# Optimization experiments

Measured on AMD Instinct MI355X. Metric: run time of the kernel, lower is better.

The kernel has to match this reference:

```python
import jax, jax.numpy as jnp
import numpy as np

N_NODES = 100000
N_EDGES = 1600000
IN_CH = 128
OUT_CH = 32
HEADS = 2
NEG_SLOPE = 0.2  # GATv2Conv default negative_slope


def setup_inputs() -> dict:
    key = jax.random.key(0)
    ks = jax.random.split(key, 6)
    x = jax.random.normal(ks[0], (N_NODES, IN_CH), dtype=jnp.float32)
    edge_index = jax.random.randint(ks[1], (2, N_EDGES), 0, N_NODES, dtype=jnp.int64)
    s_in = 1.0 / np.sqrt(IN_CH)
    Wl = jax.random.normal(ks[2], (IN_CH, HEADS * OUT_CH), dtype=jnp.float32) * s_in  # lin_l weight
    Wr = jax.random.normal(ks[3], (IN_CH, HEADS * OUT_CH), dtype=jnp.float32) * s_in  # lin_r weight
    bl = jnp.zeros((HEADS * OUT_CH,), dtype=jnp.float32)
    br = jnp.zeros((HEADS * OUT_CH,), dtype=jnp.float32)
    att = jax.random.normal(ks[4], (HEADS, OUT_CH), dtype=jnp.float32) * (1.0 / np.sqrt(OUT_CH))
    bias = jnp.zeros((OUT_CH,), dtype=jnp.float32)  # output bias (concat=False -> size out_channels)
    return {"x": x, "Wl": Wl, "bl": bl, "Wr": Wr, "br": br, "att": att, "bias": bias,
            "edge_index": edge_index}


def _gatv2_layer(x, Wl, bl, Wr, br, att, bias, edge_index):
    N = x.shape[0]
    H, C = att.shape
    # add self loops (GATv2Conv default add_self_loops=True)
    loops = jnp.arange(N, dtype=edge_index.dtype)
    src = jnp.concatenate([edge_index[0], loops])  # [E+N] message sources j
    dst = jnp.concatenate([edge_index[1], loops])  # [E+N] message targets i
    # per-node linear transforms (share_weights=False)
    xl = (x @ Wl + bl).reshape(N, H, C)
    xr = (x @ Wr + br).reshape(N, H, C)
    # GATv2 dynamic attention: a^T LeakyReLU(xl[j] + xr[i])
    h = xl[src] + xr[dst]                                   # [E, H, C]
    e = jnp.einsum('ehc,hc->eh', jax.nn.leaky_relu(h, NEG_SLOPE), att)  # [E, H]
    # segment softmax over incoming edges of each target node
    m = jax.ops.segment_max(e, dst, num_segments=N)         # [N, H]
    a = jnp.exp(e - m[dst])
    denom = jax.ops.segment_sum(a, dst, num_segments=N)     # [N, H]
    alpha = a / (denom[dst] + 1e-16)                        # [E, H]
    # weighted scatter-add of source messages
    out = jax.ops.segment_sum(alpha[:, :, None] * xl[src], dst, num_segments=N)  # [N, H, C]
    out = out.mean(axis=1) + bias                           # concat=False -> head mean
    return jax.nn.silu(out)                                 # activation='silu'


def reference(x, Wl, bl, Wr, br, att, bias, edge_index):
    return _gatv2_layer(x, Wl, bl, Wr, br, att, bias, edge_index)
```

## Files before the change

### kernel.cpp

```cpp
#include <hip/hip_runtime.h>
#include <math.h>

#define BSH 9
#define BMASK ((1 << BSH) - 1)
#define CAP 12288
#define ACH 8192

typedef unsigned int uint;
typedef __attribute__((ext_vector_type(8))) short bf16x8;
typedef __attribute__((ext_vector_type(4))) float f32x4;
typedef __attribute__((ext_vector_type(2))) float f32x2;

static __device__ __forceinline__ unsigned short f2bf(float f) {
    uint u = __float_as_uint(f);
    return (unsigned short)((u + 0x7fffu + ((u >> 16) & 1u)) >> 16);
}

static __device__ __forceinline__ bf16x8 pack8(f32x4 a, f32x4 b) {
    uint p0, p1, p2, p3;
    asm("v_cvt_pk_bf16_f32 %0, %1, %2" : "=v"(p0) : "v"(a.x), "v"(a.y));
    asm("v_cvt_pk_bf16_f32 %0, %1, %2" : "=v"(p1) : "v"(a.z), "v"(a.w));
    asm("v_cvt_pk_bf16_f32 %0, %1, %2" : "=v"(p2) : "v"(b.x), "v"(b.y));
    asm("v_cvt_pk_bf16_f32 %0, %1, %2" : "=v"(p3) : "v"(b.z), "v"(b.w));
    uint4 u = make_uint4(p0, p1, p2, p3);
    return *(bf16x8*)&u;
}

static __device__ __forceinline__ uint pk2(float a, float b) {
    uint d;
    asm("v_cvt_pk_bf16_f32 %0, %1, %2" : "=v"(d) : "v"(a), "v"(b));
    return d;
}

static __device__ __forceinline__ f32x2 dec2(uint u) {
    f32x2 r;
    r.x = __uint_as_float(u << 16);
    r.y = __uint_as_float(u & 0xffff0000u);
    return r;
}

static __device__ __forceinline__ f32x2 abs2(f32x2 h) {
    f32x2 r;
    r.x = __uint_as_float(__float_as_uint(h.x) & 0x7fffffffu);
    r.y = __uint_as_float(__float_as_uint(h.y) & 0x7fffffffu);
    return r;
}

static __device__ __forceinline__ float qsum(float p) {
    p += __uint_as_float(__builtin_amdgcn_mov_dpp(__float_as_uint(p), 0xB1, 0xF, 0xF, true));
    p += __uint_as_float(__builtin_amdgcn_mov_dpp(__float_as_uint(p), 0x4E, 0xF, 0xF, true));
    return p;
}

__global__ __launch_bounds__(256) void k_prep(const float* __restrict__ Wl,
                                              const float* __restrict__ Wr,
                                              unsigned short* __restrict__ Wt) {
    int si = blockIdx.x * 256 + threadIdx.x;
    int lo = si & 15;
    int hi = (si >> 4) & 3;
    int j  = (si >> 6) & 7;
    int ks = si >> 9;
    int n  = j * 16 + lo;
    int kb = ks * 32 + hi * 8;
    const float* Wp = (n < 64) ? (Wl + n) : (Wr + (n - 64));
    unsigned short v[8];
#pragma unroll
    for (int m = 0; m < 8; ++m)
        v[m] = f2bf(Wp[(size_t)(kb + m) * 64]);
    uint4 pk;
    pk.x = (uint)v[0] | ((uint)v[1] << 16);
    pk.y = (uint)v[2] | ((uint)v[3] << 16);
    pk.z = (uint)v[4] | ((uint)v[5] << 16);
    pk.w = (uint)v[6] | ((uint)v[7] << 16);
    *(uint4*)(Wt + (size_t)si * 8) = pk;
}

static __device__ __forceinline__ void gemm_body(
        const float* __restrict__ x, const unsigned short* __restrict__ Wt,
        const float* __restrict__ bl, const float* __restrict__ br,
        unsigned short* __restrict__ xlh, unsigned short* __restrict__ xrh, int N, int bid)
{
    const int t = threadIdx.x;
    const int base = bid * 128;
    const int w = t >> 6;
    const int lo = t & 15;
    const int hi = (t & 63) >> 4;
    int row0 = base + w * 32 + lo;
    int row1 = row0 + 16;
    const f32x4* x40 = (const f32x4*)x + (size_t)(row0 < N ? row0 : N - 1) * 32;
    const f32x4* x41 = (const f32x4*)x + (size_t)(row1 < N ? row1 : N - 1) * 32;
    const bf16x8* Wf = (const bf16x8*)Wt;

    f32x4 acc[2][8];
#pragma unroll
    for (int f = 0; f < 2; ++f)
#pragma unroll
        for (int j = 0; j < 8; ++j)
            acc[f][j] = (f32x4){0.f, 0.f, 0.f, 0.f};

#pragma unroll
    for (int ks = 0; ks < 4; ++ks) {
        int f4 = ks * 8 + hi * 2;
        int sbase = ks * 512 + hi * 16 + lo;
        bf16x8 av[2], bv[8];
        av[0] = pack8(x40[f4], x40[f4 + 1]);
        av[1] = pack8(x41[f4], x41[f4 + 1]);
#pragma unroll
        for (int j = 0; j < 8; ++j)
            bv[j] = Wf[sbase + j * 64];
#pragma unroll
        for (int f = 0; f < 2; ++f)
#pragma unroll
            for (int j = 0; j < 8; ++j)
                acc[f][j] = __builtin_amdgcn_mfma_f32_16x16x32_bf16(av[f], bv[j], acc[f][j], 0, 0, 0);
    }

    float blv[4], brv[4];
#pragma unroll
    for (int t2 = 0; t2 < 4; ++t2) {
        blv[t2] = bl[t2 * 16 + lo];
        brv[t2] = br[t2 * 16 + lo];
    }
#pragma unroll
    for (int f = 0; f < 2; ++f) {
#pragma unroll
        for (int q = 0; q < 4; ++q) {
            int row = base + w * 32 + f * 16 + hi * 4 + q;
            if (row < N) {
                size_t rb = (size_t)row * 64;
                *(uint*)(xlh + rb + 2 * lo)      = pk2(acc[f][0][q] + blv[0], acc[f][1][q] + blv[1]);
                *(uint*)(xlh + rb + 32 + 2 * lo) = pk2(acc[f][2][q] + blv[2], acc[f][3][q] + blv[3]);
                *(uint*)(xrh + rb + 2 * lo)      = pk2(acc[f][4][q] + brv[0], acc[f][5][q] + brv[1]);
                *(uint*)(xrh + rb + 32 + 2 * lo) = pk2(acc[f][6][q] + brv[2], acc[f][7][q] + brv[3]);
            }
        }
    }
}

static __device__ __forceinline__ void scatA_body(
        const int* __restrict__ ei, int* __restrict__ bcur,
        unsigned* __restrict__ pairs, int E, int T, int NB, int bid)
{
    __shared__ int h[256];
    __shared__ int basem[256];
    int b0 = bid * ACH;
    int cnt = min(ACH, T - b0);
    h[threadIdx.x] = 0;
    __syncthreads();
    for (int i = threadIdx.x; i < cnt; i += 256) {
        int t = b0 + i;
        int d = (t < E) ? ei[E + t] : (t - E);
        atomicAdd(&h[d >> BSH], 1);
    }
    __syncthreads();
    if (threadIdx.x < NB) {
        int c = h[threadIdx.x];
        basem[threadIdx.x] = c ? (threadIdx.x * CAP + atomicAdd(&bcur[threadIdx.x], c)) : 0;
    }
    __syncthreads();
    h[threadIdx.x] = 0;
    __syncthreads();
    for (int i = threadIdx.x; i < cnt; i += 256) {
        int t = b0 + i;
        int s, d;
        if (t < E) { s = ei[t]; d = ei[E + t]; } else { s = t - E; d = s; }
        int b = d >> BSH;
        int idx = atomicAdd(&h[b], 1);
        pairs[basem[b] + idx] = ((unsigned)s << BSH) | (unsigned)(d & BMASK);
    }
}

__global__ __launch_bounds__(256) void k_gs(const float* __restrict__ x,
        const unsigned short* __restrict__ Wt,
        const float* __restrict__ bl, const float* __restrict__ br,
        unsigned short* __restrict__ xlh, unsigned short* __restrict__ xrh, int N,
        const int* __restrict__ ei, int* __restrict__ bcur,
        unsigned* __restrict__ pairs, int E, int T, int NB, int SB, int R)
{
    int bid = blockIdx.x;
    int sbef = (int)(((long long)bid * SB) / R);
    int snow = (int)(((long long)(bid + 1) * SB) / R);
    if (snow > sbef)
        scatA_body(ei, bcur, pairs, E, T, NB, sbef);
    else
        gemm_body(x, Wt, bl, br, xlh, xrh, N, bid - sbef);
}

__global__ __launch_bounds__(512) void k_scatB(const unsigned* __restrict__ pairs,
                                               const int* __restrict__ bcur,
                                               int* __restrict__ src_s, int2* __restrict__ rowrng, int N) {
    __shared__ int cnt[512];
    __shared__ int sm[512];
    __shared__ int lofs[512];
    int b = blockIdx.x;
    int beg = b * CAP, end = beg + bcur[b];
    int nbase = b << BSH;
    cnt[threadIdx.x] = 0;
    __syncthreads();
    for (int i = beg + threadIdx.x; i < end; i += 512)
        atomicAdd(&cnt[pairs[i] & BMASK], 1);
    __syncthreads();
    int v = cnt[threadIdx.x];
    sm[threadIdx.x] = v;
    __syncthreads();
    int acc = v;
    for (int off = 1; off < 512; off <<= 1) {
        int t = (threadIdx.x >= off) ? sm[threadIdx.x - off] : 0;
        __syncthreads();
        acc += t;
        sm[threadIdx.x] = acc;
        __syncthreads();
    }
    int excl = acc - v;
    lofs[threadIdx.x] = excl;
    int n = nbase + threadIdx.x;
    if (n < N) rowrng[n] = make_int2(beg + excl, beg + excl + v);
    cnt[threadIdx.x] = 0;
    __syncthreads();
    for (int i = beg + threadIdx.x; i < end; i += 512) {
        unsigned p = pairs[i];
        int dl = p & BMASK;
        int idx = atomicAdd(&cnt[dl], 1);
        src_s[beg + lofs[dl] + idx] = p >> BSH;
    }
}

__global__ __launch_bounds__(256) void k_fused(const int2* __restrict__ rowrng,
        const int* __restrict__ src_s, const unsigned short* __restrict__ xlh,
        const unsigned short* __restrict__ xrh, const float* __restrict__ att,
        const float* __restrict__ bias, float* __restrict__ out, int N)
{
    int n = blockIdx.x * 32 + (threadIdx.x >> 3);
    int jf = threadIdx.x & 7;
    if (n >= N) return;
    int hsel = jf >> 2, l4 = jf & 3;
    const uint4* xl4 = (const uint4*)xlh + jf;
    f32x2 xr2[4], a06[4], a04[4];
    {
        uint4 u = ((const uint4*)xrh)[(size_t)n * 8 + jf];
        xr2[0] = dec2(u.x); xr2[1] = dec2(u.y);
        xr2[2] = dec2(u.z); xr2[3] = dec2(u.w);
        int cb = hsel * 32 + 4 * l4;
#pragma unroll
        for (int k = 0; k < 4; ++k) {
            float c0 = att[cb + k], c1 = att[cb + 16 + k];
            a06[k] = (f32x2){0.6f * c0, 0.6f * c1};
            a04[k] = (f32x2){0.4f * c0, 0.4f * c1};
        }
    }
    int2 rr = rowrng[n];
    float ssum = 0.f;
    f32x2 acc2[4] = {(f32x2){0.f,0.f}, (f32x2){0.f,0.f}, (f32x2){0.f,0.f}, (f32x2){0.f,0.f}};

#define EDGE_BODY(u)                                                      \
    {                                                                     \
        f32x2 v0 = dec2((u).x), v1 = dec2((u).y), v2 = dec2((u).z), v3 = dec2((u).w); \
        f32x2 h0 = v0 + xr2[0], h1 = v1 + xr2[1], h2 = v2 + xr2[2], h3 = v3 + xr2[3]; \
        f32x2 pa = h0 * a06[0]; pa += h1 * a06[1]; pa += h2 * a06[2]; pa += h3 * a06[3]; \
        pa += abs2(h0) * a04[0]; pa += abs2(h1) * a04[1];                 \
        pa += abs2(h2) * a04[2]; pa += abs2(h3) * a04[3];                 \
        float p = pa.x + pa.y;                                            \
        p = qsum(p);                                                      \
        float wq = __expf(p);                                             \
        ssum += wq;                                                       \
        f32x2 ws = (f32x2){wq, wq};                                       \
        acc2[0] += ws * v0; acc2[1] += ws * v1;                           \
        acc2[2] += ws * v2; acc2[3] += ws * v3;                           \
    }

    int i = rr.x;
    for (; i + 8 <= rr.y; i += 8) {
        uint4 u[8];
#pragma unroll
        for (int q = 0; q < 8; ++q)
            u[q] = xl4[((uint)src_s[i + q] << 3)];
#pragma unroll
        for (int q = 0; q < 8; ++q)
            EDGE_BODY(u[q]);
    }
    if (i + 4 <= rr.y) {
        uint4 u[4];
#pragma unroll
        for (int q = 0; q < 4; ++q)
            u[q] = xl4[((uint)src_s[i + q] << 3)];
#pragma unroll
        for (int q = 0; q < 4; ++q)
            EDGE_BODY(u[q]);
        i += 4;
    }
    for (; i < rr.y; ++i) {
        uint4 u0 = xl4[((uint)src_s[i] << 3)];
        EDGE_BODY(u0);
    }
#undef EDGE_BODY

    float inv = 1.f / ssum;
    float o[8];
#pragma unroll
    for (int q = 0; q < 4; ++q) {
        float vx = acc2[q].x * inv, vy = acc2[q].y * inv;
        o[2 * q]     = (vx + __shfl_xor(vx, 4)) * 0.5f;
        o[2 * q + 1] = (vy + __shfl_xor(vy, 4)) * 0.5f;
    }
    if (jf < 4) {
        float4 b0 = ((const float4*)bias)[l4];
        float4 b1 = *(const float4*)(bias + 16 + 4 * l4);
        float4 r0, r1;
        r0.x = o[0] + b0.x; r0.y = o[2] + b0.y; r0.z = o[4] + b0.z; r0.w = o[6] + b0.w;
        r1.x = o[1] + b1.x; r1.y = o[3] + b1.y; r1.z = o[5] + b1.z; r1.w = o[7] + b1.w;
        r0.x = r0.x / (1.f + __expf(-r0.x));
        r0.y = r0.y / (1.f + __expf(-r0.y));
        r0.z = r0.z / (1.f + __expf(-r0.z));
        r0.w = r0.w / (1.f + __expf(-r0.w));
        r1.x = r1.x / (1.f + __expf(-r1.x));
        r1.y = r1.y / (1.f + __expf(-r1.y));
        r1.z = r1.z / (1.f + __expf(-r1.z));
        r1.w = r1.w / (1.f + __expf(-r1.w));
        ((float4*)out)[(size_t)n * 8 + l4]     = r0;
        ((float4*)out)[(size_t)n * 8 + 4 + l4] = r1;
    }
}

extern "C" void kernel_launch(void* const* d_in, const int* in_sizes, int n_in,
                              void* d_out, int out_size, void* d_ws, size_t ws_size,
                              hipStream_t stream) {
    const float* x    = (const float*)d_in[0];
    const float* Wl   = (const float*)d_in[1];
    const float* bl   = (const float*)d_in[2];
    const float* Wr   = (const float*)d_in[3];
    const float* br   = (const float*)d_in[4];
    const float* att  = (const float*)d_in[5];
    const float* bias = (const float*)d_in[6];
    const int*   ei   = (const int*)d_in[7];
    float* out = (float*)d_out;

    const int N = in_sizes[0] / 128;
    const int E = in_sizes[7] / 2;
    const int T = E + N;
    const int NB = (N + (1 << BSH) - 1) >> BSH;

    char* p = (char*)d_ws;
    auto take = [&](size_t bytes) {
        char* r = p;
        p += (bytes + 255) & ~(size_t)255;
        return r;
    };
    unsigned short* xlh = (unsigned short*)take((size_t)N * 64 * 2);
    unsigned short* xrh = (unsigned short*)take((size_t)N * 64 * 2);
    unsigned* pairs  = (unsigned*)take((size_t)NB * CAP * 4);
    int*      src_s  = (int*)take((size_t)NB * CAP * 4);
    int2*     rowrng = (int2*)take((size_t)N * 8);
    int*      bcur   = (int*)take((size_t)NB * 4);
    unsigned short* Wt = (unsigned short*)take((size_t)128 * 128 * 2);

    const int GB = (N + 127) / 128;
    const int SB = (T + ACH - 1) / ACH;
    const int R  = GB + SB;
    hipMemsetAsync(bcur, 0, (size_t)NB * 4, stream);
    k_prep <<<8,             256, 0, stream>>>(Wl, Wr, Wt);
    k_gs   <<<R,             256, 0, stream>>>(x, Wt, bl, br, xlh, xrh, N,
                                               ei, bcur, pairs, E, T, NB, SB, R);
    k_scatB<<<NB,            512, 0, stream>>>(pairs, bcur, src_s, rowrng, N);
    k_fused<<<(N + 31) / 32, 256, 0, stream>>>(rowrng, src_s, xlh, xrh, att, bias, out, N);
}
```

Measured before the change: 110.4 us.

## Split fused GEMM/scatter kernel, shrink scatter chunks, deepen edge-gather unroll

Separates the combined GEMM+bucket-scatter kernel back into two launches: the GEMM gets 512-thread blocks with one 16-row MFMA tile per wave, and the scatter gets smaller per-block chunks (2048 instead of 8192 edges) for more blocks. The fused attention kernel's edge loop adds a 16-wide gather unroll to keep more loads in flight. The aim is better parallelism in the scatter and more memory-level parallelism in the gather. In exchange it adds a kernel launch, loses the GEMM/scatter overlap inside a single grid, puts more contention on the global bucket counters, and raises register pressure in the edge loop.

Result: slower. 123.3 us (+11.6%).

```diff
diff --git a/kernel.cpp b/kernel.cpp
--- a/kernel.cpp
+++ b/kernel.cpp
@@ -4,7 +4,7 @@
 #define BSH 9
 #define BMASK ((1 << BSH) - 1)
 #define CAP 12288
-#define ACH 8192
+#define ACH 2048
 
 typedef unsigned int uint;
 typedef __attribute__((ext_vector_type(8))) short bf16x8;
@@ -75,44 +75,37 @@
     *(uint4*)(Wt + (size_t)si * 8) = pk;
 }
 
-static __device__ __forceinline__ void gemm_body(
+__global__ __launch_bounds__(512) void k_gemm(
         const float* __restrict__ x, const unsigned short* __restrict__ Wt,
         const float* __restrict__ bl, const float* __restrict__ br,
-        unsigned short* __restrict__ xlh, unsigned short* __restrict__ xrh, int N, int bid)
+        unsigned short* __restrict__ xlh, unsigned short* __restrict__ xrh, int N)
 {
     const int t = threadIdx.x;
-    const int base = bid * 128;
+    const int base = blockIdx.x * 128;
     const int w = t >> 6;
     const int lo = t & 15;
     const int hi = (t & 63) >> 4;
-    int row0 = base + w * 32 + lo;
-    int row1 = row0 + 16;
-    const f32x4* x40 = (const f32x4*)x + (size_t)(row0 < N ? row0 : N - 1) * 32;
-    const f32x4* x41 = (const f32x4*)x + (size_t)(row1 < N ? row1 : N - 1) * 32;
+    int rowa = base + w * 16 + lo;
+    const f32x4* x4 = (const f32x4*)x + (size_t)(rowa < N ? rowa : N - 1) * 32;
     const bf16x8* Wf = (const bf16x8*)Wt;
 
-    f32x4 acc[2][8];
-#pragma unroll
-    for (int f = 0; f < 2; ++f)
-#pragma unroll
-        for (int j = 0; j < 8; ++j)
-            acc[f][j] = (f32x4){0.f, 0.f, 0.f, 0.f};
+    f32x4 acc[8];
+#pragma unroll
+    for (int j = 0; j < 8; ++j)
+        acc[j] = (f32x4){0.f, 0.f, 0.f, 0.f};
 
 #pragma unroll
     for (int ks = 0; ks < 4; ++ks) {
         int f4 = ks * 8 + hi * 2;
         int sbase = ks * 512 + hi * 16 + lo;
-        bf16x8 av[2], bv[8];
-        av[0] = pack8(x40[f4], x40[f4 + 1]);
-        av[1] = pack8(x41[f4], x41[f4 + 1]);
+        bf16x8 av = pack8(x4[f4], x4[f4 + 1]);
+        bf16x8 bv[8];
 #pragma unroll
         for (int j = 0; j < 8; ++j)
             bv[j] = Wf[sbase + j * 64];
 #pragma unroll
-        for (int f = 0; f < 2; ++f)
-#pragma unroll
-            for (int j = 0; j < 8; ++j)
-                acc[f][j] = __builtin_amdgcn_mfma_f32_16x16x32_bf16(av[f], bv[j], acc[f][j], 0, 0, 0);
+        for (int j = 0; j < 8; ++j)
+            acc[j] = __builtin_amdgcn_mfma_f32_16x16x32_bf16(av, bv[j], acc[j], 0, 0, 0);
     }
 
     float blv[4], brv[4];
@@ -122,28 +115,23 @@
         brv[t2] = br[t2 * 16 + lo];
     }
 #pragma unroll
-    for (int f = 0; f < 2; ++f) {
-#pragma unroll
-        for (int q = 0; q < 4; ++q) {
-            int row = base + w * 32 + f * 16 + hi * 4 + q;
-            if (row < N) {
-                size_t rb = (size_t)row * 64;
-                *(uint*)(xlh + rb + 2 * lo)      = pk2(acc[f][0][q] + blv[0], acc[f][1][q] + blv[1]);
-                *(uint*)(xlh + rb + 32 + 2 * lo) = pk2(acc[f][2][q] + blv[2], acc[f][3][q] + blv[3]);
-                *(uint*)(xrh + rb + 2 * lo)      = pk2(acc[f][4][q] + brv[0], acc[f][5][q] + brv[1]);
-                *(uint*)(xrh + rb + 32 + 2 * lo) = pk2(acc[f][6][q] + brv[2], acc[f][7][q] + brv[3]);
-            }
+    for (int q = 0; q < 4; ++q) {
+        int row = base + w * 16 + hi * 4 + q;
+        if (row < N) {
+            size_t rb = (size_t)row * 64;
+            *(uint*)(xlh + rb + 2 * lo)      = pk2(acc[0][q] + blv[0], acc[1][q] + blv[1]);
+            *(uint*)(xlh + rb + 32 + 2 * lo) = pk2(acc[2][q] + blv[2], acc[3][q] + blv[3]);
+            *(uint*)(xrh + rb + 2 * lo)      = pk2(acc[4][q] + brv[0], acc[5][q] + brv[1]);
+            *(uint*)(xrh + rb + 32 + 2 * lo) = pk2(acc[6][q] + brv[2], acc[7][q] + brv[3]);
         }
     }
 }
 
-static __device__ __forceinline__ void scatA_body(
-        const int* __restrict__ ei, int* __restrict__ bcur,
-        unsigned* __restrict__ pairs, int E, int T, int NB, int bid)
-{
+__global__ __launch_bounds__(256) void k_scatA(const int* __restrict__ ei, int* __restrict__ bcur,
+                                               unsigned* __restrict__ pairs, int E, int T, int NB) {
     __shared__ int h[256];
     __shared__ int basem[256];
-    int b0 = bid * ACH;
+    int b0 = blockIdx.x * ACH;
     int cnt = min(ACH, T - b0);
     h[threadIdx.x] = 0;
     __syncthreads();
@@ -168,22 +156,6 @@
         int idx = atomicAdd(&h[b], 1);
         pairs[basem[b] + idx] = ((unsigned)s << BSH) | (unsigned)(d & BMASK);
     }
-}
-
-__global__ __launch_bounds__(256) void k_gs(const float* __restrict__ x,
-        const unsigned short* __restrict__ Wt,
-        const float* __restrict__ bl, const float* __restrict__ br,
-        unsigned short* __restrict__ xlh, unsigned short* __restrict__ xrh, int N,
-        const int* __restrict__ ei, int* __restrict__ bcur,
-        unsigned* __restrict__ pairs, int E, int T, int NB, int SB, int R)
-{
-    int bid = blockIdx.x;
-    int sbef = (int)(((long long)bid * SB) / R);
-    int snow = (int)(((long long)(bid + 1) * SB) / R);
-    if (snow > sbef)
-        scatA_body(ei, bcur, pairs, E, T, NB, sbef);
-    else
-        gemm_body(x, Wt, bl, br, xlh, xrh, N, bid - sbef);
 }
 
 __global__ __launch_bounds__(512) void k_scatB(const unsigned* __restrict__ pairs,
@@ -269,7 +241,16 @@
     }
 
     int i = rr.x;
-    for (; i + 8 <= rr.y; i += 8) {
+    for (; i + 16 <= rr.y; i += 16) {
+        uint4 u[16];
+#pragma unroll
+        for (int q = 0; q < 16; ++q)
+            u[q] = xl4[((uint)src_s[i + q] << 3)];
+#pragma unroll
+        for (int q = 0; q < 16; ++q)
+            EDGE_BODY(u[q]);
+    }
+    if (i + 8 <= rr.y) {
         uint4 u[8];
 #pragma unroll
         for (int q = 0; q < 8; ++q)
@@ -277,6 +258,7 @@
 #pragma unroll
         for (int q = 0; q < 8; ++q)
             EDGE_BODY(u[q]);
+        i += 8;
     }
     if (i + 4 <= rr.y) {
         uint4 u[4];
@@ -353,13 +335,10 @@
     int*      bcur   = (int*)take((size_t)NB * 4);
     unsigned short* Wt = (unsigned short*)take((size_t)128 * 128 * 2);
 
-    const int GB = (N + 127) / 128;
-    const int SB = (T + ACH - 1) / ACH;
-    const int R  = GB + SB;
     hipMemsetAsync(bcur, 0, (size_t)NB * 4, stream);
-    k_prep <<<8,             256, 0, stream>>>(Wl, Wr, Wt);
-    k_gs   <<<R,             256, 0, stream>>>(x, Wt, bl, br, xlh, xrh, N,
-                                               ei, bcur, pairs, E, T, NB, SB, R);
-    k_scatB<<<NB,            512, 0, stream>>>(pairs, bcur, src_s, rowrng, N);
-    k_fused<<<(N + 31) / 32, 256, 0, stream>>>(rowrng, src_s, xlh, xrh, att, bias, out, N);
-}
+    k_prep <<<8,                   256, 0, stream>>>(Wl, Wr, Wt);
+    k_gemm <<<(N + 127) / 128,     512, 0, stream>>>(x, Wt, bl, br, xlh, xrh, N);
+    k_scatA<<<(T + ACH - 1) / ACH, 256, 0, stream>>>(ei, bcur, pairs, E, T, NB);
+    k_scatB<<<NB,                  512, 0, stream>>>(pairs, bcur, src_s, rowrng, N);
+    k_fused<<<(N + 31) / 32,       256, 0, stream>>>(rowrng, src_s, xlh, xrh, att, bias, out, N);
+}
```
